# Optimization experiments

Measured on AMD Instinct MI355X. Metric: run time of the kernel, lower is better.

## Reference

```python
import jax, jax.numpy as jnp
import numpy as np

D = 1024          # input_dim == output_dim == key_size
SLOTS = 128       # memory_slots
HID = 128         # write_heads hidden width
EPS = 1e-5        # LayerNorm eps (torch default)
WRITE_STRENGTH = 0.1


def _layernorm(x, g, b):
    mu = jnp.mean(x, axis=-1, keepdims=True)
    var = jnp.var(x, axis=-1, keepdims=True)
    return (x - mu) * jax.lax.rsqrt(var + EPS) * g + b


def setup_inputs() -> dict:
    key = jax.random.key(0)
    ks = jax.random.split(key, 12)
    B, S = 8, 4096
    xavier = float(np.sqrt(6.0 / (SLOTS + D)))
    return {
        "x": jax.random.normal(ks[0], (B, S, D), dtype=jnp.float32),
        "keys": jax.random.uniform(ks[1], (SLOTS, D), jnp.float32, -xavier, xavier),
        # original inits values to zeros but they become nonzero after writes; use small randn for a meaningful read
        "values": jax.random.normal(ks[2], (SLOTS, D), dtype=jnp.float32) * 0.02,
        "temperature": jnp.array([0.1], dtype=jnp.float32),
        "W1": jax.random.normal(ks[3], (D, HID), dtype=jnp.float32) * 0.02,
        "b1": jnp.zeros((HID,), jnp.float32),
        "W2": jax.random.normal(ks[4], (HID, SLOTS), dtype=jnp.float32) * 0.02,
        "b2": jnp.zeros((SLOTS,), jnp.float32),
        "Wf": jax.random.normal(ks[5], (2 * D, D), dtype=jnp.float32) * 0.02,
        "bf": jnp.zeros((D,), jnp.float32),
        "ln1_g": jnp.ones((D,), jnp.float32),
        "ln1_b": jnp.zeros((D,), jnp.float32),
        "Wo": jax.random.normal(ks[6], (D, D), dtype=jnp.float32) * 0.02,
        "bo": jnp.zeros((D,), jnp.float32),
        "ln2_g": jnp.ones((D,), jnp.float32),
        "ln2_b": jnp.zeros((D,), jnp.float32),
    }


def reference(x, keys, values, temperature, W1, b1, W2, b2, Wf, bf,
              ln1_g, ln1_b, Wo, bo, ln2_g, ln2_b):
    identity = x
    # proj_in is Identity since input_dim == output_dim
    q = x.reshape(-1, D)                                     # [N, D]
    # --- memory read: content-addressed softmax attention over SLOTS ---
    temp = jnp.clip(temperature, 1e-6, None)                 # clamp(min=1e-6)
    attn = jax.nn.softmax(q @ keys.T / temp, axis=-1)        # [N, SLOTS]
    mem_read = (attn @ values).reshape(x.shape)              # [B, S, D]
    # --- memory write (detached state update in the original) ---
    ww = jax.nn.sigmoid(jax.nn.gelu(q @ W1 + b1, approximate=False) @ W2 + b2)  # [N, SLOTS]
    new_values = values + WRITE_STRENGTH * (ww.T @ q)        # [SLOTS, D]
    # --- fusion + LN + Linear (+Dropout in eval mode = identity) ---
    fused = jnp.concatenate([x, mem_read], axis=-1) @ Wf + bf
    out = _layernorm(fused, ln1_g, ln1_b) @ Wo + bo
    # residual + post norm
    out = _layernorm(out + identity, ln2_g, ln2_b)
    return out, new_values
```

## Files before the change

kernel.cpp:

```cpp
#include <hip/hip_runtime.h>
#include <stdint.h>
#include <math.h>

typedef float f32x4 __attribute__((ext_vector_type(4)));
typedef __bf16 bf16x8_t __attribute__((ext_vector_type(8)));
typedef unsigned short us8 __attribute__((ext_vector_type(8)));
typedef unsigned short us4 __attribute__((ext_vector_type(4)));
typedef unsigned int u32;

__device__ __forceinline__ unsigned short f2bf(float f) {
  union { float f; uint32_t u; } v; v.f = f;
  uint32_t u = v.u;
  uint32_t r = (u + 0x7fffu + ((u >> 16) & 1u)) >> 16;
  return (unsigned short)r;
}
__device__ __forceinline__ float bf2f(unsigned short h) {
  union { uint32_t u; float f; } v; v.u = ((uint32_t)h) << 16;
  return v.f;
}
__device__ __forceinline__ f32x4 mfma16(us8 a, us8 b, f32x4 c) {
  return __builtin_amdgcn_mfma_f32_16x16x32_bf16(
      __builtin_bit_cast(bf16x8_t, a), __builtin_bit_cast(bf16x8_t, b), c, 0, 0, 0);
}
__device__ __forceinline__ void gl16(const void* g, void* l) {
  __builtin_amdgcn_global_load_lds(
      (const __attribute__((address_space(1))) u32*)g,
      (__attribute__((address_space(3))) u32*)l, 16, 0, 0);
}


__device__ __forceinline__ void tr_tile(
    const float* __restrict__ src, unsigned short* __restrict__ dst,
    int C, int dstride, int tile, int t)
{
  __shared__ unsigned short X[64][68];
  int tpr = C >> 6;
  int tr = tile / tpr, tc = tile % tpr;
  int r = t >> 2, c0 = (t & 3) * 16;
  const float* sp = src + (size_t)(tr * 64 + r) * C + tc * 64 + c0;
  #pragma unroll
  for (int q = 0; q < 4; ++q) {
    f32x4 v = *(const f32x4*)(sp + q * 4);
    us4 o;
    #pragma unroll
    for (int e = 0; e < 4; ++e) o[e] = f2bf(v[e]);
    *(us4*)&X[r][c0 + q * 4] = o;
  }
  __syncthreads();
  int o = t >> 2, k0 = (t & 3) * 16;
  us8 w0, w1;
  #pragma unroll
  for (int e = 0; e < 8; ++e) { w0[e] = X[k0 + e][o]; w1[e] = X[k0 + 8 + e][o]; }
  unsigned short* dp = dst + (size_t)(tc * 64 + o) * dstride + (size_t)tr * 64 + k0;
  *(us8*)dp = w0;
  *(us8*)(dp + 8) = w1;
}

__global__ __launch_bounds__(256) void k_prep_all(
    const float* __restrict__ Wf, const float* __restrict__ W1,
    const float* __restrict__ W2, const float* __restrict__ keys,
    const float* __restrict__ values,
    unsigned short* __restrict__ wfb, unsigned short* __restrict__ shW,
    unsigned short* __restrict__ klw1, unsigned short* __restrict__ w2t,
    unsigned short* __restrict__ valB)
{
  int b = blockIdx.x, t = threadIdx.x;
  if (b < 256)       { tr_tile(Wf,            wfb,            1024, 1152, b,       t); return; }
  if (b < 512)       { tr_tile(Wf + 1048576,  shW,            1024, 1024, b - 256, t); return; }
  if (b < 544)       { tr_tile(W1,            klw1 + 131072,  128,  1024, b - 512, t); return; }
  if (b < 548)       { tr_tile(W2,            w2t,            128,  128,  b - 544, t); return; }
  int i = (b - 548) * 256 + t;
  if (i < 131072) { klw1[i] = f2bf(keys[i]); return; }
  i -= 131072;
  valB[i] = f2bf(values[i]);
}

__global__ __launch_bounds__(256) void k_tr(
    const float* __restrict__ src, unsigned short* __restrict__ dst,
    int C, int dstride)
{
  tr_tile(src, dst, C, dstride, blockIdx.x, threadIdx.x);
}

template<int KTOT, int MT, int NTILES, int EPI, int KSPLIT = KTOT>
__global__ __launch_bounds__(512, 2) void k_gemm(
    const unsigned short* __restrict__ A, int astride,
    const unsigned short* __restrict__ A2, int astride2,
    const unsigned short* __restrict__ B,
    const float* __restrict__ bias,
    unsigned short* __restrict__ outB, float* __restrict__ outF,
    int ostride, int ocol,
    const unsigned short* __restrict__ residB)
{
  constexpr int NT = KTOT / 64;
  constexpr int AHW = MT * 64;
  constexpr int BUFHW = AHW + 16384;
  constexpr int AJ = MT / 64;
  constexpr int IFR = MT / 32;
  __shared__ __align__(16) unsigned short L[2 * BUFHW];

  int t = threadIdx.x;
  int bid = blockIdx.x;
  int logical;
  if (gridDim.x & 7) {
    logical = bid;
  } else {
    int cpx = gridDim.x >> 3;
    logical = (bid & 7) * cpx + (bid >> 3);
  }
  int m0 = (logical / NTILES) * MT, n0 = (logical % NTILES) * 256;

  int srow = t >> 3;
  int gslot = (t & 7) ^ (srow & 7);

  int w = t >> 6, l = t & 63, g = l >> 4, lc = l & 15;
  int wm = w >> 2, wn = w & 3;

  f32x4 acc[IFR][4] = {};

  auto stage = [&](int p, int kt) {
    int koff = kt * 64;
    const unsigned short* Ap = A; int astr = astride;
    if constexpr (KSPLIT < KTOT) {
      if (koff >= KSPLIT) { Ap = A2; astr = astride2; koff -= KSPLIT; }
    }
    int offa = koff + gslot * 8;
    int offb = kt * 64 + gslot * 8;
    #pragma unroll
    for (int j = 0; j < AJ; ++j)
      gl16(Ap + (size_t)(m0 + j * 64 + srow) * astr + offa,
           L + p * BUFHW + (j * 64 + srow) * 64 + (t & 7) * 8);
    #pragma unroll
    for (int j = 0; j < 4; ++j)
      gl16(B + (size_t)(n0 + j * 64 + srow) * KTOT + offb,
           L + p * BUFHW + AHW + (j * 64 + srow) * 64 + (t & 7) * 8);
  };

  stage(0, 0);
  if (NT > 1) stage(1, 1);

  for (int kt = 0; kt < NT; ++kt) {
    int p = kt & 1;
    if (kt + 1 < NT) {
      if constexpr (AJ + 4 == 6) asm volatile("s_waitcnt vmcnt(6)" ::: "memory");
      else                       asm volatile("s_waitcnt vmcnt(8)" ::: "memory");
    } else {
      asm volatile("s_waitcnt vmcnt(0)" ::: "memory");
    }
    __builtin_amdgcn_s_barrier();

    const unsigned short* Ab = L + p * BUFHW;
    const unsigned short* Bb = L + p * BUFHW + AHW;
    #pragma unroll
    for (int ks = 0; ks < 2; ++ks) {
      us8 av[IFR], bv[4];
      #pragma unroll
      for (int i = 0; i < IFR; ++i) {
        int row = wm * (MT / 2) + i * 16 + lc;
        av[i] = *(const us8*)(Ab + row * 64 + (((ks * 4 + g) ^ (lc & 7)) * 8));
      }
      #pragma unroll
      for (int j = 0; j < 4; ++j) {
        int row = wn * 64 + j * 16 + lc;
        bv[j] = *(const us8*)(Bb + row * 64 + (((ks * 4 + g) ^ (lc & 7)) * 8));
      }
      __builtin_amdgcn_s_setprio(1);
      #pragma unroll
      for (int i = 0; i < IFR; ++i)
        #pragma unroll
        for (int j = 0; j < 4; ++j)
          acc[i][j] = mfma16(av[i], bv[j], acc[i][j]);
      __builtin_amdgcn_s_setprio(0);
    }
    __builtin_amdgcn_s_barrier();
    if (kt + 2 < NT) stage(p, kt + 2);
  }

  float bv4[4];
  if constexpr (EPI == 0 || EPI == 5) {
    #pragma unroll
    for (int jn = 0; jn < 4; ++jn) bv4[jn] = bias[n0 + wn * 64 + jn * 16 + lc];
  }
  #pragma unroll
  for (int i = 0; i < IFR; ++i) {
    #pragma unroll
    for (int jj = 0; jj < 4; ++jj) {
      int row = m0 + wm * (MT / 2) + i * 16 + g * 4 + jj;
      #pragma unroll
      for (int jn = 0; jn < 4; ++jn) {
        int col = n0 + wn * 64 + jn * 16 + lc;
        float v = acc[i][jn][jj];
        if constexpr (EPI == 0 || EPI == 5) v += bv4[jn];
        if constexpr (EPI == 5) v += bf2f(residB[(size_t)row * 1024 + col]);
        if constexpr (EPI == 4) {
          outB[(size_t)col * 1152 + 1024 + row] = f2bf(v);
        } else {
          size_t oa = (size_t)row * ostride + ocol + col;
          if constexpr (EPI == 0 || EPI == 5) outB[oa] = f2bf(v);
          else                                outF[oa] = v;
        }
      }
    }
  }
}

__global__ __launch_bounds__(512, 4) void k_logx(
    const float* __restrict__ x, const unsigned short* __restrict__ klw1,
    unsigned short* __restrict__ xb, float* __restrict__ lg)
{
  constexpr int NT = 16;
  __shared__ __align__(16) unsigned short Al[2][4096];
  __shared__ __align__(16) unsigned short Bl[2][16384];

  int t = threadIdx.x;
  int bid = blockIdx.x;
  int cpx = gridDim.x >> 3;
  int logical = (bid & 7) * cpx + (bid >> 3);
  int m0 = logical * 64;

  int ar = t >> 3, aq = t & 7;
  int adst = ar * 64 + ((aq ^ (ar & 7)) * 8);
  const float* axp = x + (size_t)(m0 + ar) * 1024 + aq * 8;
  unsigned short* xbp = xb + (size_t)(m0 + ar) * 1024 + aq * 8;

  int srow = t >> 3;
  int gslot = (t & 7) ^ (srow & 7);

  int w = t >> 6, l = t & 63, g = l >> 4, lc = l & 15;
  int wm = w >> 2, wn = w & 3;

  f32x4 acc[2][4] = {};
  f32x4 a0, a1;

  auto loadA = [&](int kt) {
    a0 = *(const f32x4*)(axp + kt * 64);
    a1 = *(const f32x4*)(axp + kt * 64 + 4);
  };
  auto stageB = [&](int p, int kt) {
    #pragma unroll
    for (int j = 0; j < 4; ++j)
      gl16(klw1 + (size_t)(j * 64 + srow) * 1024 + kt * 64 + gslot * 8,
           &Bl[p][(j * 64 + srow) * 64 + (t & 7) * 8]);
  };

  loadA(0);
  stageB(0, 0);

  for (int kt = 0; kt < NT; ++kt) {
    int cur = kt & 1;
    us8 av8;
    #pragma unroll
    for (int e = 0; e < 4; ++e) { av8[e] = f2bf(a0[e]); av8[e + 4] = f2bf(a1[e]); }
    *(us8*)(xbp + kt * 64) = av8;
    *(us8*)&Al[cur][adst] = av8;
    __syncthreads();
    if (kt + 1 < NT) {
      loadA(kt + 1);
      stageB(cur ^ 1, kt + 1);
    }
    #pragma unroll
    for (int ks = 0; ks < 2; ++ks) {
      us8 af[2], bf[4];
      #pragma unroll
      for (int i = 0; i < 2; ++i) {
        int row = wm * 32 + i * 16 + lc;
        af[i] = *(const us8*)&Al[cur][row * 64 + (((ks * 4 + g) ^ (lc & 7)) * 8)];
      }
      #pragma unroll
      for (int j = 0; j < 4; ++j) {
        int row = wn * 64 + j * 16 + lc;
        bf[j] = *(const us8*)&Bl[cur][row * 64 + (((ks * 4 + g) ^ (lc & 7)) * 8)];
      }
      #pragma unroll
      for (int i = 0; i < 2; ++i)
        #pragma unroll
        for (int j = 0; j < 4; ++j)
          acc[i][j] = mfma16(af[i], bf[j], acc[i][j]);
    }
    __syncthreads();
  }

  #pragma unroll
  for (int i = 0; i < 2; ++i)
    #pragma unroll
    for (int jj = 0; jj < 4; ++jj) {
      int row = m0 + wm * 32 + i * 16 + g * 4 + jj;
      #pragma unroll
      for (int jn = 0; jn < 4; ++jn) {
        int col = wn * 64 + jn * 16 + lc;
        lg[(size_t)row * 256 + col] = acc[i][jn][jj];
      }
    }
}

__global__ __launch_bounds__(256) void k_smx(
    const float* __restrict__ lg, const float* __restrict__ b1,
    const float* __restrict__ b2, const float* __restrict__ temp,
    const unsigned short* __restrict__ w2t,
    unsigned short* __restrict__ attn, unsigned short* __restrict__ ww)
{
  __shared__ float lgs[16][260];
  __shared__ unsigned short hl[16][136];
  int t = threadIdx.x;
  int row0 = blockIdx.x * 16;

  {
    int r = t >> 4, c0 = (t & 15) * 16;
    const float* p = lg + (size_t)(row0 + r) * 256 + c0;
    #pragma unroll
    for (int q = 0; q < 4; ++q)
      *(f32x4*)&lgs[r][c0 + q * 4] = *(const f32x4*)(p + q * 4);
  }
  __syncthreads();

  {
    int r = t >> 4, sub = t & 15;
    float invt = 1.f / fmaxf(temp[0], 1e-6f);
    float vals[8]; float m = -3.4e38f;
    #pragma unroll
    for (int i = 0; i < 8; ++i) { vals[i] = lgs[r][sub * 8 + i]; m = fmaxf(m, vals[i]); }
    m = fmaxf(m, __shfl_xor(m, 1)); m = fmaxf(m, __shfl_xor(m, 2));
    m = fmaxf(m, __shfl_xor(m, 4)); m = fmaxf(m, __shfl_xor(m, 8));
    float ev[8]; float s = 0.f;
    #pragma unroll
    for (int i = 0; i < 8; ++i) { ev[i] = __expf((vals[i] - m) * invt); s += ev[i]; }
    s += __shfl_xor(s, 1); s += __shfl_xor(s, 2);
    s += __shfl_xor(s, 4); s += __shfl_xor(s, 8);
    float rinv = 1.f / s;
    us8 av;
    #pragma unroll
    for (int i = 0; i < 8; ++i) av[i] = f2bf(ev[i] * rinv);
    *(us8*)(attn + (size_t)(row0 + r) * 128 + sub * 8) = av;
    #pragma unroll
    for (int i = 0; i < 8; ++i) {
      float v = lgs[r][128 + sub * 8 + i] + b1[sub * 8 + i];
      v = 0.5f * v * (1.f + erff(v * 0.70710678118654752f));
      hl[r][sub * 8 + i] = f2bf(v);
    }
  }
  __syncthreads();

  int w = t >> 6, l = t & 63, g = l >> 4, lc = l & 15;
  int q2 = w * 2;
  f32x4 acc[2] = {};
  #pragma unroll
  for (int ks = 0; ks < 4; ++ks) {
    us8 a = *(const us8*)&hl[lc][ks * 32 + g * 8];
    #pragma unroll
    for (int i = 0; i < 2; ++i) {
      us8 b = *(const us8*)(w2t + (size_t)((q2 + i) * 16 + lc) * 128 + ks * 32 + g * 8);
      acc[i] = mfma16(a, b, acc[i]);
    }
  }
  #pragma unroll
  for (int i = 0; i < 2; ++i) {
    int col = (q2 + i) * 16 + lc;
    float bb = b2[col];
    #pragma unroll
    for (int j = 0; j < 4; ++j) {
      int r = row0 + g * 4 + j;
      float v = acc[i][j] + bb;
      v = 1.f / (1.f + __expf(-v));
      ww[(size_t)r * 128 + col] = f2bf(v);
    }
  }
}

__global__ __launch_bounds__(256) void k_wv(
    const unsigned short* __restrict__ xb, const unsigned short* __restrict__ ww,
    float* __restrict__ partials)
{
  __shared__ unsigned short wwT[128][40];
  __shared__ unsigned short xT[128][40];
  int t = threadIdx.x;
  int chunk = blockIdx.x >> 3;
  int dt0 = (blockIdx.x & 7) * 128;
  int w = t >> 6, l = t & 63, g = l >> 4, lc = l & 15;
  f32x4 acc[2][8] = {};
  int nn = t >> 3, e0 = (t & 7) * 16;

  for (int ks = 0; ks < 32; ++ks) {
    int n0 = chunk * 1024 + ks * 32;
    __syncthreads();
    {
      us8 v0 = *(const us8*)(ww + (size_t)(n0 + nn) * 128 + e0);
      us8 v1 = *(const us8*)(ww + (size_t)(n0 + nn) * 128 + e0 + 8);
      #pragma unroll
      for (int i = 0; i < 8; ++i) { wwT[e0 + i][nn] = v0[i]; wwT[e0 + 8 + i][nn] = v1[i]; }
      const unsigned short* xp = xb + (size_t)(n0 + nn) * 1024 + dt0 + e0;
      us8 x0 = *(const us8*)xp;
      us8 x1 = *(const us8*)(xp + 8);
      #pragma unroll
      for (int i = 0; i < 8; ++i) { xT[e0 + i][nn] = x0[i]; xT[e0 + 8 + i][nn] = x1[i]; }
    }
    __syncthreads();
    us8 bfr[8];
    #pragma unroll
    for (int i = 0; i < 8; ++i) bfr[i] = *(const us8*)&xT[i * 16 + lc][g * 8];
    #pragma unroll
    for (int st = 0; st < 2; ++st) {
      us8 a = *(const us8*)&wwT[(w * 2 + st) * 16 + lc][g * 8];
      #pragma unroll
      for (int i = 0; i < 8; ++i) acc[st][i] = mfma16(a, bfr[i], acc[st][i]);
    }
  }
  float* p = partials + (size_t)chunk * 131072;
  #pragma unroll
  for (int st = 0; st < 2; ++st)
    #pragma unroll
    for (int i = 0; i < 8; ++i)
      #pragma unroll
      for (int j = 0; j < 4; ++j) {
        int s = (w * 2 + st) * 16 + g * 4 + j;
        p[s * 1024 + dt0 + i * 16 + lc] = acc[st][i][j];
      }
}

__global__ __launch_bounds__(256) void k_red(
    const float* __restrict__ values, const float* __restrict__ partials,
    float* __restrict__ outv)
{
  int i = blockIdx.x * 256 + threadIdx.x;
  float s = 0.f;
  #pragma unroll
  for (int c = 0; c < 32; ++c) s += partials[(size_t)c * 131072 + i];
  outv[i] = values[i] + 0.1f * s;
}

__global__ __launch_bounds__(256) void k_ln1(
    unsigned short* __restrict__ fb,
    const float* __restrict__ g, const float* __restrict__ b)
{
  int w = threadIdx.x >> 6, l = threadIdx.x & 63;
  int row = blockIdx.x * 4 + w;
  unsigned short* p = fb + (size_t)row * 1024 + l * 16;
  us8 v0 = *(const us8*)p;
  us8 v1 = *(const us8*)(p + 8);
  float vf[16];
  float s = 0.f, sq = 0.f;
  #pragma unroll
  for (int e = 0; e < 8; ++e) { vf[e] = bf2f(v0[e]); vf[e + 8] = bf2f(v1[e]); }
  #pragma unroll
  for (int e = 0; e < 16; ++e) { s += vf[e]; sq += vf[e] * vf[e]; }
  #pragma unroll
  for (int msk = 1; msk < 64; msk <<= 1) {
    s += __shfl_xor(s, msk); sq += __shfl_xor(sq, msk);
  }
  float mu = s * (1.f / 1024.f);
  float rs = rsqrtf(sq * (1.f / 1024.f) - mu * mu + 1e-5f);
  float gv[16], bv[16];
  #pragma unroll
  for (int q = 0; q < 4; ++q) {
    *(f32x4*)&gv[q * 4] = *(const f32x4*)(g + l * 16 + q * 4);
    *(f32x4*)&bv[q * 4] = *(const f32x4*)(b + l * 16 + q * 4);
  }
  us8 o0, o1;
  #pragma unroll
  for (int e = 0; e < 8; ++e) {
    o0[e] = f2bf((vf[e] - mu) * rs * gv[e] + bv[e]);
    o1[e] = f2bf((vf[e + 8] - mu) * rs * gv[e + 8] + bv[e + 8]);
  }
  *(us8*)p = o0;
  *(us8*)(p + 8) = o1;
}

__global__ __launch_bounds__(256) void k_ln2(
    const unsigned short* __restrict__ tp,
    const float* __restrict__ g, const float* __restrict__ b,
    float* __restrict__ out)
{
  int w = threadIdx.x >> 6, l = threadIdx.x & 63;
  int row = blockIdx.x * 4 + w;
  size_t base = (size_t)row * 1024 + l * 16;
  us8 t0 = *(const us8*)(tp + base);
  us8 t1 = *(const us8*)(tp + base + 8);
  float vf[16];
  #pragma unroll
  for (int e = 0; e < 8; ++e) { vf[e] = bf2f(t0[e]); vf[e + 8] = bf2f(t1[e]); }
  float s = 0.f, sq = 0.f;
  #pragma unroll
  for (int e = 0; e < 16; ++e) { s += vf[e]; sq += vf[e] * vf[e]; }
  #pragma unroll
  for (int msk = 1; msk < 64; msk <<= 1) {
    s += __shfl_xor(s, msk); sq += __shfl_xor(sq, msk);
  }
  float mu = s * (1.f / 1024.f);
  float rs = rsqrtf(sq * (1.f / 1024.f) - mu * mu + 1e-5f);
  #pragma unroll
  for (int q = 0; q < 4; ++q) {
    f32x4 gv = *(const f32x4*)(g + l * 16 + q * 4);
    f32x4 bv = *(const f32x4*)(b + l * 16 + q * 4);
    f32x4 o;
    #pragma unroll
    for (int e = 0; e < 4; ++e)
      o[e] = (vf[q * 4 + e] - mu) * rs * gv[e] + bv[e];
    *(f32x4*)(out + base + q * 4) = o;
  }
}

extern "C" void kernel_launch(void* const* d_in, const int* in_sizes, int n_in,
                              void* d_out, int out_size, void* d_ws, size_t ws_size,
                              hipStream_t stream) {
  const float* x      = (const float*)d_in[0];
  const float* keys   = (const float*)d_in[1];
  const float* values = (const float*)d_in[2];
  const float* temp   = (const float*)d_in[3];
  const float* W1     = (const float*)d_in[4];
  const float* b1     = (const float*)d_in[5];
  const float* W2     = (const float*)d_in[6];
  const float* b2     = (const float*)d_in[7];
  const float* Wf     = (const float*)d_in[8];
  const float* bfp    = (const float*)d_in[9];
  const float* ln1g   = (const float*)d_in[10];
  const float* ln1b   = (const float*)d_in[11];
  const float* Wo     = (const float*)d_in[12];
  const float* bo     = (const float*)d_in[13];
  const float* ln2g   = (const float*)d_in[14];
  const float* ln2b   = (const float*)d_in[15];

  char* ws = (char*)d_ws;
  unsigned short* wfb   = (unsigned short*)(ws + 0);
  unsigned short* shW   = (unsigned short*)(ws + 2359296);
  unsigned short* klw1  = (unsigned short*)(ws + 4456448);
  unsigned short* w2t   = (unsigned short*)(ws + 4980736);
  unsigned short* valB  = (unsigned short*)(ws + 5013504);
  unsigned short* attn  = (unsigned short*)(ws + 5275648);
  unsigned short* ww    = (unsigned short*)(ws + 13664256);
  float* lg             = (float*)(ws + 22052864);
  float* partials       = (float*)(ws + 22052864);
  unsigned short* tprime = (unsigned short*)(ws + 22052864);

  unsigned short* fb    = (unsigned short*)d_out;
  unsigned short* xb    = (unsigned short*)((char*)d_out + 67108864);
  float* out            = (float*)d_out;
  float* newvals        = (float*)((char*)d_out + 134217728);

  k_prep_all<<<1572, 256, 0, stream>>>(Wf, W1, W2, keys, values,
                                       wfb, shW, klw1, w2t, valB);

  k_gemm<1024, 128, 4, 4><<<4, 512, 0, stream>>>(
      valB, 1024, nullptr, 0, shW, nullptr, wfb, nullptr, 0, 0, nullptr);
  k_tr<<<256, 256, 0, stream>>>(Wo, shW, 1024, 1024);

  k_logx<<<512, 512, 0, stream>>>(x, klw1, xb, lg);
  k_smx<<<2048, 256, 0, stream>>>(lg, b1, b2, temp, w2t, attn, ww);

  k_wv<<<256, 256, 0, stream>>>(xb, ww, partials);
  k_red<<<512, 256, 0, stream>>>(values, partials, newvals);

  k_gemm<1152, 256, 4, 0, 1024><<<512, 512, 0, stream>>>(
      xb, 1024, attn, 128, wfb, bfp, fb, nullptr, 1024, 0, nullptr);
  k_ln1<<<8192, 256, 0, stream>>>(fb, ln1g, ln1b);

  k_gemm<1024, 256, 4, 5><<<512, 512, 0, stream>>>(
      fb, 1024, nullptr, 0, shW, bo, tprime, nullptr, 1024, 0, xb);
  k_ln2<<<8192, 256, 0, stream>>>(tprime, ln2g, ln2b, out);
}
```

Baseline: 388.1 us.

## Fuse softmax, GELU and write-head MLP into logits kernel; fold Wo transpose into prep

The logits GEMM kernel now computes the attention softmax, GELU of the hidden layer, the small W2 MFMA and the sigmoid in its epilogue via shared memory, writing bf16 attn and ww directly. This removes the fp32 logits buffer round trip through global memory and the separate k_smx launch. The Wo transpose is merged into the prep kernel into its own buffer, removing another launch and the aliasing of shW. The epilogue adds block barriers and leaves half the waves idle during softmax.

```diff
diff --git a/kernel.cpp b/kernel.cpp
--- a/kernel.cpp
+++ b/kernel.cpp
@@ -57,29 +57,23 @@
 }
 
 __global__ __launch_bounds__(256) void k_prep_all(
-    const float* __restrict__ Wf, const float* __restrict__ W1,
-    const float* __restrict__ W2, const float* __restrict__ keys,
-    const float* __restrict__ values,
+    const float* __restrict__ Wf, const float* __restrict__ Wo,
+    const float* __restrict__ W1, const float* __restrict__ W2,
+    const float* __restrict__ keys, const float* __restrict__ values,
     unsigned short* __restrict__ wfb, unsigned short* __restrict__ shW,
-    unsigned short* __restrict__ klw1, unsigned short* __restrict__ w2t,
-    unsigned short* __restrict__ valB)
+    unsigned short* __restrict__ woT, unsigned short* __restrict__ klw1,
+    unsigned short* __restrict__ w2t, unsigned short* __restrict__ valB)
 {
   int b = blockIdx.x, t = threadIdx.x;
-  if (b < 256)       { tr_tile(Wf,            wfb,            1024, 1152, b,       t); return; }
-  if (b < 512)       { tr_tile(Wf + 1048576,  shW,            1024, 1024, b - 256, t); return; }
-  if (b < 544)       { tr_tile(W1,            klw1 + 131072,  128,  1024, b - 512, t); return; }
-  if (b < 548)       { tr_tile(W2,            w2t,            128,  128,  b - 544, t); return; }
-  int i = (b - 548) * 256 + t;
+  if (b < 256)  { tr_tile(Wf,           wfb,           1024, 1152, b,       t); return; }
+  if (b < 512)  { tr_tile(Wf + 1048576, shW,           1024, 1024, b - 256, t); return; }
+  if (b < 768)  { tr_tile(Wo,           woT,           1024, 1024, b - 512, t); return; }
+  if (b < 800)  { tr_tile(W1,           klw1 + 131072, 128,  1024, b - 768, t); return; }
+  if (b < 804)  { tr_tile(W2,           w2t,           128,  128,  b - 800, t); return; }
+  int i = (b - 804) * 256 + t;
   if (i < 131072) { klw1[i] = f2bf(keys[i]); return; }
   i -= 131072;
   valB[i] = f2bf(values[i]);
-}
-
-__global__ __launch_bounds__(256) void k_tr(
-    const float* __restrict__ src, unsigned short* __restrict__ dst,
-    int C, int dstride)
-{
-  tr_tile(src, dst, C, dstride, blockIdx.x, threadIdx.x);
 }
 
 template<int KTOT, int MT, int NTILES, int EPI, int KSPLIT = KTOT>
@@ -206,11 +200,15 @@
 
 __global__ __launch_bounds__(512, 4) void k_logx(
     const float* __restrict__ x, const unsigned short* __restrict__ klw1,
-    unsigned short* __restrict__ xb, float* __restrict__ lg)
+    const float* __restrict__ b1, const float* __restrict__ b2,
+    const float* __restrict__ temp, const unsigned short* __restrict__ w2t,
+    unsigned short* __restrict__ xb, unsigned short* __restrict__ attn,
+    unsigned short* __restrict__ ww)
 {
   constexpr int NT = 16;
-  __shared__ __align__(16) unsigned short Al[2][4096];
-  __shared__ __align__(16) unsigned short Bl[2][16384];
+  __shared__ __align__(16) char LR[81920];
+  unsigned short* Al = (unsigned short*)LR;
+  unsigned short* Bl = (unsigned short*)(LR + 16384);
 
   int t = threadIdx.x;
   int bid = blockIdx.x;
@@ -240,7 +238,7 @@
     #pragma unroll
     for (int j = 0; j < 4; ++j)
       gl16(klw1 + (size_t)(j * 64 + srow) * 1024 + kt * 64 + gslot * 8,
-           &Bl[p][(j * 64 + srow) * 64 + (t & 7) * 8]);
+           &Bl[p * 16384 + (j * 64 + srow) * 64 + (t & 7) * 8]);
   };
 
   loadA(0);
@@ -252,7 +250,7 @@
     #pragma unroll
     for (int e = 0; e < 4; ++e) { av8[e] = f2bf(a0[e]); av8[e + 4] = f2bf(a1[e]); }
     *(us8*)(xbp + kt * 64) = av8;
-    *(us8*)&Al[cur][adst] = av8;
+    *(us8*)&Al[cur * 4096 + adst] = av8;
     __syncthreads();
     if (kt + 1 < NT) {
       loadA(kt + 1);
@@ -264,12 +262,12 @@
       #pragma unroll
       for (int i = 0; i < 2; ++i) {
         int row = wm * 32 + i * 16 + lc;
-        af[i] = *(const us8*)&Al[cur][row * 64 + (((ks * 4 + g) ^ (lc & 7)) * 8)];
+        af[i] = *(const us8*)&Al[cur * 4096 + row * 64 + (((ks * 4 + g) ^ (lc & 7)) * 8)];
       }
       #pragma unroll
       for (int j = 0; j < 4; ++j) {
         int row = wn * 64 + j * 16 + lc;
-        bf[j] = *(const us8*)&Bl[cur][row * 64 + (((ks * 4 + g) ^ (lc & 7)) * 8)];
+        bf[j] = *(const us8*)&Bl[cur * 16384 + row * 64 + (((ks * 4 + g) ^ (lc & 7)) * 8)];
       }
       #pragma unroll
       for (int i = 0; i < 2; ++i)
@@ -280,88 +278,99 @@
     __syncthreads();
   }
 
-  #pragma unroll
-  for (int i = 0; i < 2; ++i)
-    #pragma unroll
-    for (int jj = 0; jj < 4; ++jj) {
-      int row = m0 + wm * 32 + i * 16 + g * 4 + jj;
+  float* rm = (float*)LR;
+  float* sm = (float*)(LR + 512);
+  unsigned short* hb = (unsigned short*)(LR + 16384);
+  float invt = 1.f / fmaxf(temp[0], 1e-6f);
+
+  if (wn < 2) {
+    #pragma unroll
+    for (int i = 0; i < 2; ++i)
+      #pragma unroll
+      for (int jj = 0; jj < 4; ++jj) {
+        float mx = fmaxf(fmaxf(acc[i][0][jj], acc[i][1][jj]),
+                         fmaxf(acc[i][2][jj], acc[i][3][jj]));
+        mx = fmaxf(mx, __shfl_xor(mx, 1)); mx = fmaxf(mx, __shfl_xor(mx, 2));
+        mx = fmaxf(mx, __shfl_xor(mx, 4)); mx = fmaxf(mx, __shfl_xor(mx, 8));
+        if (lc == 0) rm[(wm * 32 + i * 16 + g * 4 + jj) * 2 + wn] = mx;
+      }
+  } else {
+    #pragma unroll
+    for (int i = 0; i < 2; ++i)
+      #pragma unroll
+      for (int jj = 0; jj < 4; ++jj) {
+        int r = wm * 32 + i * 16 + g * 4 + jj;
+        #pragma unroll
+        for (int jn = 0; jn < 4; ++jn) {
+          int colh = (wn - 2) * 64 + jn * 16 + lc;
+          float v = acc[i][jn][jj] + b1[colh];
+          v = 0.5f * v * (1.f + erff(v * 0.70710678118654752f));
+          hb[r * 128 + (((colh >> 3) ^ (r & 7)) * 8) + (colh & 7)] = f2bf(v);
+        }
+      }
+  }
+  __syncthreads();
+
+  if (wn < 2) {
+    #pragma unroll
+    for (int i = 0; i < 2; ++i)
+      #pragma unroll
+      for (int jj = 0; jj < 4; ++jj) {
+        int r = wm * 32 + i * 16 + g * 4 + jj;
+        float m = fmaxf(rm[r * 2], rm[r * 2 + 1]);
+        float s = 0.f;
+        #pragma unroll
+        for (int jn = 0; jn < 4; ++jn) {
+          float e = __expf((acc[i][jn][jj] - m) * invt);
+          acc[i][jn][jj] = e;
+          s += e;
+        }
+        s += __shfl_xor(s, 1); s += __shfl_xor(s, 2);
+        s += __shfl_xor(s, 4); s += __shfl_xor(s, 8);
+        if (lc == 0) sm[r * 2 + wn] = s;
+      }
+  }
+  __syncthreads();
+
+  if (wn < 2) {
+    #pragma unroll
+    for (int i = 0; i < 2; ++i)
+      #pragma unroll
+      for (int jj = 0; jj < 4; ++jj) {
+        int r = wm * 32 + i * 16 + g * 4 + jj;
+        float rinv = 1.f / (sm[r * 2] + sm[r * 2 + 1]);
+        #pragma unroll
+        for (int jn = 0; jn < 4; ++jn) {
+          int col = wn * 64 + jn * 16 + lc;
+          attn[(size_t)(m0 + r) * 128 + col] = f2bf(acc[i][jn][jj] * rinv);
+        }
+      }
+  }
+
+  {
+    int band = w & 3, ch0 = (w >> 2) * 64;
+    int arow = band * 16 + lc;
+    f32x4 acc2[4] = {};
+    #pragma unroll
+    for (int ks = 0; ks < 4; ++ks) {
+      us8 a = *(const us8*)&hb[arow * 128 + (((ks * 4 + g) ^ (arow & 7)) * 8)];
       #pragma unroll
       for (int jn = 0; jn < 4; ++jn) {
-        int col = wn * 64 + jn * 16 + lc;
-        lg[(size_t)row * 256 + col] = acc[i][jn][jj];
-      }
-    }
-}
-
-__global__ __launch_bounds__(256) void k_smx(
-    const float* __restrict__ lg, const float* __restrict__ b1,
-    const float* __restrict__ b2, const float* __restrict__ temp,
-    const unsigned short* __restrict__ w2t,
-    unsigned short* __restrict__ attn, unsigned short* __restrict__ ww)
-{
-  __shared__ float lgs[16][260];
-  __shared__ unsigned short hl[16][136];
-  int t = threadIdx.x;
-  int row0 = blockIdx.x * 16;
-
-  {
-    int r = t >> 4, c0 = (t & 15) * 16;
-    const float* p = lg + (size_t)(row0 + r) * 256 + c0;
-    #pragma unroll
-    for (int q = 0; q < 4; ++q)
-      *(f32x4*)&lgs[r][c0 + q * 4] = *(const f32x4*)(p + q * 4);
-  }
-  __syncthreads();
-
-  {
-    int r = t >> 4, sub = t & 15;
-    float invt = 1.f / fmaxf(temp[0], 1e-6f);
-    float vals[8]; float m = -3.4e38f;
-    #pragma unroll
-    for (int i = 0; i < 8; ++i) { vals[i] = lgs[r][sub * 8 + i]; m = fmaxf(m, vals[i]); }
-    m = fmaxf(m, __shfl_xor(m, 1)); m = fmaxf(m, __shfl_xor(m, 2));
-    m = fmaxf(m, __shfl_xor(m, 4)); m = fmaxf(m, __shfl_xor(m, 8));
-    float ev[8]; float s = 0.f;
-    #pragma unroll
-    for (int i = 0; i < 8; ++i) { ev[i] = __expf((vals[i] - m) * invt); s += ev[i]; }
-    s += __shfl_xor(s, 1); s += __shfl_xor(s, 2);
-    s += __shfl_xor(s, 4); s += __shfl_xor(s, 8);
-    float rinv = 1.f / s;
-    us8 av;
-    #pragma unroll
-    for (int i = 0; i < 8; ++i) av[i] = f2bf(ev[i] * rinv);
-    *(us8*)(attn + (size_t)(row0 + r) * 128 + sub * 8) = av;
-    #pragma unroll
-    for (int i = 0; i < 8; ++i) {
-      float v = lgs[r][128 + sub * 8 + i] + b1[sub * 8 + i];
-      v = 0.5f * v * (1.f + erff(v * 0.70710678118654752f));
-      hl[r][sub * 8 + i] = f2bf(v);
-    }
-  }
-  __syncthreads();
-
-  int w = t >> 6, l = t & 63, g = l >> 4, lc = l & 15;
-  int q2 = w * 2;
-  f32x4 acc[2] = {};
-  #pragma unroll
-  for (int ks = 0; ks < 4; ++ks) {
-    us8 a = *(const us8*)&hl[lc][ks * 32 + g * 8];
-    #pragma unroll
-    for (int i = 0; i < 2; ++i) {
-      us8 b = *(const us8*)(w2t + (size_t)((q2 + i) * 16 + lc) * 128 + ks * 32 + g * 8);
-      acc[i] = mfma16(a, b, acc[i]);
-    }
-  }
-  #pragma unroll
-  for (int i = 0; i < 2; ++i) {
-    int col = (q2 + i) * 16 + lc;
-    float bb = b2[col];
-    #pragma unroll
-    for (int j = 0; j < 4; ++j) {
-      int r = row0 + g * 4 + j;
-      float v = acc[i][j] + bb;
-      v = 1.f / (1.f + __expf(-v));
-      ww[(size_t)r * 128 + col] = f2bf(v);
+        us8 b = *(const us8*)(w2t + (size_t)(ch0 + jn * 16 + lc) * 128 + ks * 32 + g * 8);
+        acc2[jn] = mfma16(a, b, acc2[jn]);
+      }
+    }
+    #pragma unroll
+    for (int jn = 0; jn < 4; ++jn) {
+      int col = ch0 + jn * 16 + lc;
+      float bb = b2[col];
+      #pragma unroll
+      for (int jj = 0; jj < 4; ++jj) {
+        int r = band * 16 + g * 4 + jj;
+        float v = acc2[jn][jj] + bb;
+        v = 1.f / (1.f + __expf(-v));
+        ww[(size_t)(m0 + r) * 128 + col] = f2bf(v);
+      }
     }
   }
 }
@@ -521,29 +530,27 @@
   char* ws = (char*)d_ws;
   unsigned short* wfb   = (unsigned short*)(ws + 0);
   unsigned short* shW   = (unsigned short*)(ws + 2359296);
-  unsigned short* klw1  = (unsigned short*)(ws + 4456448);
-  unsigned short* w2t   = (unsigned short*)(ws + 4980736);
-  unsigned short* valB  = (unsigned short*)(ws + 5013504);
-  unsigned short* attn  = (unsigned short*)(ws + 5275648);
-  unsigned short* ww    = (unsigned short*)(ws + 13664256);
-  float* lg             = (float*)(ws + 22052864);
-  float* partials       = (float*)(ws + 22052864);
-  unsigned short* tprime = (unsigned short*)(ws + 22052864);
+  unsigned short* woT   = (unsigned short*)(ws + 4456448);
+  unsigned short* klw1  = (unsigned short*)(ws + 6553600);
+  unsigned short* w2t   = (unsigned short*)(ws + 7077888);
+  unsigned short* valB  = (unsigned short*)(ws + 7110656);
+  unsigned short* attn  = (unsigned short*)(ws + 7372800);
+  unsigned short* ww    = (unsigned short*)(ws + 15761408);
+  float* partials       = (float*)(ws + 24150016);
+  unsigned short* tprime = (unsigned short*)(ws + 24150016);
 
   unsigned short* fb    = (unsigned short*)d_out;
   unsigned short* xb    = (unsigned short*)((char*)d_out + 67108864);
   float* out            = (float*)d_out;
   float* newvals        = (float*)((char*)d_out + 134217728);
 
-  k_prep_all<<<1572, 256, 0, stream>>>(Wf, W1, W2, keys, values,
-                                       wfb, shW, klw1, w2t, valB);
+  k_prep_all<<<1828, 256, 0, stream>>>(Wf, Wo, W1, W2, keys, values,
+                                       wfb, shW, woT, klw1, w2t, valB);
 
   k_gemm<1024, 128, 4, 4><<<4, 512, 0, stream>>>(
       valB, 1024, nullptr, 0, shW, nullptr, wfb, nullptr, 0, 0, nullptr);
-  k_tr<<<256, 256, 0, stream>>>(Wo, shW, 1024, 1024);
-
-  k_logx<<<512, 512, 0, stream>>>(x, klw1, xb, lg);
-  k_smx<<<2048, 256, 0, stream>>>(lg, b1, b2, temp, w2t, attn, ww);
+
+  k_logx<<<512, 512, 0, stream>>>(x, klw1, b1, b2, temp, w2t, xb, attn, ww);
 
   k_wv<<<256, 256, 0, stream>>>(xb, ww, partials);
   k_red<<<512, 256, 0, stream>>>(values, partials, newvals);
@@ -553,6 +560,6 @@
   k_ln1<<<8192, 256, 0, stream>>>(fb, ln1g, ln1b);
 
   k_gemm<1024, 256, 4, 5><<<512, 512, 0, stream>>>(
-      fb, 1024, nullptr, 0, shW, bo, tprime, nullptr, 1024, 0, xb);
+      fb, 1024, nullptr, 0, woT, bo, tprime, nullptr, 1024, 0, xb);
   k_ln2<<<8192, 256, 0, stream>>>(tprime, ln2g, ln2b, out);
 }
```

Result: faster. 368.5 us (-5.0%).
